# Performance work log

Measured on AMD Instinct MI355X. Metric: run time of the kernel, lower is better.

Reference implementation:

```python
import jax, jax.numpy as jnp
import numpy as np
from jax import lax

ALPHA = 2.0          # HausdorffDistanceLoss alpha
W_CE, W_BD, W_HD = 1.0, 0.5, 0.5   # combined-loss weights
NOSEED = 1e4         # sentinel 1D distance for lines with no seed pixel (>> max real distance)


def _sq_dt_binary(seed):
    """Exact squared 1D distance (along last axis) to nearest True pixel. seed: [..., L] bool."""
    L = seed.shape[-1]
    idx = jnp.arange(L, dtype=jnp.int32)
    left = lax.cummax(jnp.where(seed, idx, -1), axis=seed.ndim - 1)
    right = lax.cummin(jnp.where(seed, idx, 2 * L), axis=seed.ndim - 1, reverse=True)
    dl = jnp.where(left >= 0, (idx - left).astype(jnp.float32), jnp.float32(NOSEED))
    dr = jnp.where(right < 2 * L, (right - idx).astype(jnp.float32), jnp.float32(NOSEED))
    d = jnp.minimum(dl, dr)
    return d * d


def _sq_dt_general(f):
    """d[j] = min_y f[..., y] + (j - y)^2 along last axis (lower envelope, brute force via scan)."""
    L = f.shape[-1]
    idx = jnp.arange(L, dtype=f.dtype)
    fm = jnp.moveaxis(f, -1, 0)  # [L, ...]
    def step(carry, inp):
        fy, y = inp
        cand = fy[..., None] + (idx - y) ** 2  # [..., L]
        return jnp.minimum(carry, cand), None
    init = jnp.full(f.shape, jnp.float32(1e18), f.dtype)
    d, _ = lax.scan(step, init, (fm, idx))
    return d


def edt(seed):
    """Exact 2D Euclidean distance to nearest True pixel. seed: [..., H, W] bool.
    Equivalent to scipy.ndimage.distance_transform_edt(~seed)... i.e. scipy's
    distance_transform_edt(m) == edt(m == 0)."""
    g = jnp.swapaxes(_sq_dt_binary(jnp.swapaxes(seed, -1, -2)), -1, -2)  # pass along H
    return jnp.sqrt(_sq_dt_general(g))  # pass along W


def setup_inputs() -> dict:
    key = jax.random.key(0)
    k1, k2 = jax.random.split(key)
    pred = jax.random.normal(k1, (8, 4, 256, 256), dtype=jnp.float32)
    target = jax.random.randint(k2, (8, 256, 256), 0, 4).astype(jnp.int64)
    return {"pred": pred, "target": target}


def reference(pred, target):
    N, C, H, W = pred.shape
    tgt = target.astype(jnp.int32)

    # --- CrossEntropyLoss (mean over N,H,W) ---
    log_p = jax.nn.log_softmax(pred, axis=1)
    ce = -jnp.mean(jnp.take_along_axis(log_p, tgt[:, None, :, :], axis=1))

    p = jnp.exp(log_p)  # softmax probabilities

    # one-hot target as bool mask [N, C, H, W]
    m = tgt[:, None, :, :] == jnp.arange(C, dtype=jnp.int32)[None, :, None, None]

    # signed distance map: distance_transform_edt(~m) - distance_transform_edt(m)
    dist_to_fg = edt(m)    # == scipy distance_transform_edt(~m): dist to nearest foreground
    dist_to_bg = edt(~m)   # == scipy distance_transform_edt(m):  dist to nearest background
    signed_dm = dist_to_fg - dist_to_bg  # negative inside object

    # --- BoundaryLoss (exclude background channel 0) ---
    bd = jnp.mean(jnp.sum(p[:, 1:] * signed_dm[:, 1:], axis=(2, 3)))

    # --- HausdorffDistanceLoss (exclude background) ---
    dt_gt = dist_to_fg[:, 1:]                     # distance_transform_edt(gt_mask == 0)
    pred_seed = lax.stop_gradient(p[:, 1:]) >= 0.5  # threshold is detached in torch code
    dt_pred = edt(pred_seed)                      # distance_transform_edt(pred < 0.5)
    gt_f = m[:, 1:].astype(p.dtype)
    term1 = jnp.mean(p[:, 1:] * dt_gt ** ALPHA, axis=(2, 3))   # per (n, c) spatial means
    term2 = jnp.mean(gt_f * dt_pred ** ALPHA, axis=(2, 3))
    hd = (jnp.sum(term1) + jnp.sum(term2)) / (2 * N * (C - 1))

    total = W_CE * ce + W_BD * bd + W_HD * hd
    return total, ce, bd, hd
```

## Files before the change

kernel.cpp:

```cpp
#include <hip/hip_runtime.h>

#define NB 8
#define NC 4
#define HH 256
#define WW 256
#define HW_ (HH * WW)
#define NSL 24
#define CT 8
#define NT (WW/CT)
#define HP (HH + 1)
#define GRIDN (NSL * NT)

typedef unsigned long long u64;

__global__ __launch_bounds__(256) void k_softmax_ce(
    const float* __restrict__ pred, const int* __restrict__ tgt,
    float* __restrict__ pbuf, u64* __restrict__ rmT, u64* __restrict__ rmP,
    double* __restrict__ pce) {
  int b = blockIdx.x;
  int n = b >> 8, h = b & (HH - 1);
  int w = threadIdx.x;
  size_t base = (size_t)n * NC * HW_ + (size_t)h * WW + w;
  float x0 = pred[base];
  float x1 = pred[base + HW_];
  float x2 = pred[base + 2 * HW_];
  float x3 = pred[base + 3 * HW_];
  float mx = fmaxf(fmaxf(x0, x1), fmaxf(x2, x3));
  float e0 = __expf(x0 - mx), e1 = __expf(x1 - mx);
  float e2 = __expf(x2 - mx), e3 = __expf(x3 - mx);
  float sum = e0 + e1 + e2 + e3;
  float lse = mx + __logf(sum);
  int t = tgt[(size_t)n * HW_ + h * WW + w];
  float xt = (t == 0) ? x0 : (t == 1) ? x1 : (t == 2) ? x2 : x3;
  float ce = lse - xt;
  float inv = 1.0f / sum;
  float p1 = e1 * inv, p2 = e2 * inv, p3 = e3 * inv;
  size_t pb = ((size_t)(n * 3)) * HW_ + (size_t)h * WW + w;
  pbuf[pb]           = p1;
  pbuf[pb + HW_]     = p2;
  pbuf[pb + 2 * HW_] = p3;
  u64 bT1 = __ballot(t == 1), bP1 = __ballot(p1 >= 0.5f);
  u64 bT2 = __ballot(t == 2), bP2 = __ballot(p2 >= 0.5f);
  u64 bT3 = __ballot(t == 3), bP3 = __ballot(p3 >= 0.5f);
  int v = threadIdx.x >> 6;
  if ((threadIdx.x & 63) == 0) {
    size_t mi = ((size_t)(n * 3) * HH + h) * 4 + v;
    rmT[mi]                      = bT1;  rmP[mi]                      = bP1;
    rmT[mi + (size_t)HH * 4]     = bT2;  rmP[mi + (size_t)HH * 4]     = bP2;
    rmT[mi + (size_t)2 * HH * 4] = bT3;  rmP[mi + (size_t)2 * HH * 4] = bP3;
  }
  double cd = (double)ce;
  #pragma unroll
  for (int o = 32; o > 0; o >>= 1) cd += __shfl_down(cd, o, 64);
  if ((threadIdx.x & 63) == 0) pce[(b << 2) | v] = cd;
}

template<int WORD>
__device__ __forceinline__ int nsb_left(u64 m0, u64 m1, u64 m2, u64 m3, int bit) {
  u64 cur = (WORD == 0) ? m0 : (WORD == 1) ? m1 : (WORD == 2) ? m2 : m3;
  u64 below = cur & ((bit == 63) ? ~0ull : ((1ull << (bit + 1)) - 1ull));
  if (below) return bit - (63 - (int)__builtin_clzll(below));
  if constexpr (WORD >= 1) {
    u64 x = (WORD == 1) ? m0 : (WORD == 2) ? m1 : m2;
    if (x) return bit + 1 + (int)__builtin_clzll(x);
  }
  if constexpr (WORD >= 2) {
    u64 x = (WORD == 2) ? m0 : m1;
    if (x) return bit + 65 + (int)__builtin_clzll(x);
  }
  if constexpr (WORD >= 3) {
    if (m0) return bit + 129 + (int)__builtin_clzll(m0);
  }
  return 10000;
}

template<int WORD>
__device__ __forceinline__ int nsb_right(u64 m0, u64 m1, u64 m2, u64 m3, int bit) {
  u64 cur = (WORD == 0) ? m0 : (WORD == 1) ? m1 : (WORD == 2) ? m2 : m3;
  u64 above = cur & (~0ull << bit);
  if (above) return (int)__builtin_ctzll(above) - bit;
  if constexpr (WORD <= 2) {
    u64 x = (WORD == 0) ? m1 : (WORD == 1) ? m2 : m3;
    if (x) return 64 + (int)__builtin_ctzll(x) - bit;
  }
  if constexpr (WORD <= 1) {
    u64 x = (WORD == 0) ? m2 : m3;
    if (x) return 128 + (int)__builtin_ctzll(x) - bit;
  }
  if constexpr (WORD == 0) {
    if (m3) return 192 + (int)__builtin_ctzll(m3) - bit;
  }
  return 10000;
}

template<int WORD>
__device__ __forceinline__ void filltile(
    u64 t0, u64 t1, u64 t2, u64 t3, u64 p0, u64 p1, u64 p2, u64 p3,
    int h, int bit0, float gF[CT][HP], float gB[CT][HP], float gQ[CT][HP],
    unsigned char gtb[CT][HH + 4]) {
  u64 b0 = ~t0, b1 = ~t1, b2 = ~t2, b3 = ~t3;
  u64 curT = (WORD == 0) ? t0 : (WORD == 1) ? t1 : (WORD == 2) ? t2 : t3;
  u64 curP = (WORD == 0) ? p0 : (WORD == 1) ? p1 : (WORD == 2) ? p2 : p3;
  int dF[CT], dB[CT], dQ[CT];
  int lF = nsb_left<WORD>(t0, t1, t2, t3, bit0);
  int lB = nsb_left<WORD>(b0, b1, b2, b3, bit0);
  int lP = nsb_left<WORD>(p0, p1, p2, p3, bit0);
  #pragma unroll
  for (int wi = 0; wi < CT; ++wi) {
    int bit = bit0 + wi;
    int sF = (int)((curT >> bit) & 1ull);
    int sP = (int)((curP >> bit) & 1ull);
    if (wi > 0) {
      lF = sF ? 0 : min(lF + 1, 10000);
      lB = sF ? min(lB + 1, 10000) : 0;
      lP = sP ? 0 : min(lP + 1, 10000);
    }
    dF[wi] = lF; dB[wi] = lB; dQ[wi] = lP;
  }
  int rF = nsb_right<WORD>(t0, t1, t2, t3, bit0 + CT - 1);
  int rB = nsb_right<WORD>(b0, b1, b2, b3, bit0 + CT - 1);
  int rP = nsb_right<WORD>(p0, p1, p2, p3, bit0 + CT - 1);
  #pragma unroll
  for (int wi = CT - 1; wi >= 0; --wi) {
    int bit = bit0 + wi;
    int sF = (int)((curT >> bit) & 1ull);
    int sP = (int)((curP >> bit) & 1ull);
    if (wi < CT - 1) {
      rF = sF ? 0 : min(rF + 1, 10000);
      rB = sF ? min(rB + 1, 10000) : 0;
      rP = sP ? 0 : min(rP + 1, 10000);
    }
    int vF = min(dF[wi], rF), vB = min(dB[wi], rB), vQ = min(dQ[wi], rP);
    gF[wi][h] = (float)(vF * vF);
    gB[wi][h] = (float)(vB * vB);
    gQ[wi][h] = (float)(vQ * vQ);
    gtb[wi][h] = (unsigned char)sF;
  }
}

__global__ __launch_bounds__(256) void k_env(
    const u64* __restrict__ rmT, const u64* __restrict__ rmP,
    const float* __restrict__ pbuf, double* __restrict__ part) {
  __shared__ float gF[CT][HP];
  __shared__ float gB[CT][HP];
  __shared__ float gQ[CT][HP];
  __shared__ float pp[CT][HP];
  __shared__ unsigned char gtb[CT][HH + 4];
  __shared__ double sbuf[12];
  int tid = threadIdx.x;
  int s  = blockIdx.x;
  int w0 = blockIdx.y * CT;
  int h  = tid;
  {
    size_t mi = ((size_t)s * HH + h) * 4;
    const ulonglong2* pT = (const ulonglong2*)(rmT + mi);
    const ulonglong2* pP = (const ulonglong2*)(rmP + mi);
    ulonglong2 a0 = pT[0], a1 = pT[1];
    ulonglong2 c0 = pP[0], c1 = pP[1];
    const float* prow = pbuf + (size_t)s * HW_ + (size_t)h * WW + w0;
    float4 pa = *(const float4*)prow;
    float4 pc = *(const float4*)(prow + 4);
    pp[0][h] = pa.x; pp[1][h] = pa.y; pp[2][h] = pa.z; pp[3][h] = pa.w;
    pp[4][h] = pc.x; pp[5][h] = pc.y; pp[6][h] = pc.z; pp[7][h] = pc.w;
    int bit0 = w0 & 63;
    switch (w0 >> 6) {
      case 0: filltile<0>(a0.x,a0.y,a1.x,a1.y,c0.x,c0.y,c1.x,c1.y,h,bit0,gF,gB,gQ,gtb); break;
      case 1: filltile<1>(a0.x,a0.y,a1.x,a1.y,c0.x,c0.y,c1.x,c1.y,h,bit0,gF,gB,gQ,gtb); break;
      case 2: filltile<2>(a0.x,a0.y,a1.x,a1.y,c0.x,c0.y,c1.x,c1.y,h,bit0,gF,gB,gQ,gtb); break;
      default: filltile<3>(a0.x,a0.y,a1.x,a1.y,c0.x,c0.y,c1.x,c1.y,h,bit0,gF,gB,gQ,gtb); break;
    }
  }
  __syncthreads();
  int wi = tid & (CT - 1);
  int hg = tid >> 3;
  double a_bd = 0.0, a_t1 = 0.0, a_t2 = 0.0;
  for (int k = 0; k < 8; ++k) {
    int h2 = hg * 8 + k;
    float mF = gF[wi][h2], mB = gB[wi][h2], mQ = gQ[wi][h2];
    for (int r = 1; r < HH; r += 4) {
      float rr = (float)(r * r);
      if (rr >= mF && rr >= mB && rr >= mQ) break;
      #pragma unroll
      for (int q = 0; q < 4; ++q) {
        int rq = r + q;
        float rrq = (float)(rq * rq);
        int u = h2 - rq, d = h2 + rq;
        if (u >= 0) {
          float fF = gF[wi][u], fB = gB[wi][u], fQ = gQ[wi][u];
          mF = fminf(mF, fF + rrq);
          mB = fminf(mB, fB + rrq);
          mQ = fminf(mQ, fQ + rrq);
        }
        if (d < HH) {
          float fF = gF[wi][d], fB = gB[wi][d], fQ = gQ[wi][d];
          mF = fminf(mF, fF + rrq);
          mB = fminf(mB, fB + rrq);
          mQ = fminf(mQ, fQ + rrq);
        }
      }
    }
    float dfg = sqrtf(mF), dbg = sqrtf(mB), dpr = sqrtf(mQ);
    float p  = pp[wi][h2];
    float gt = (float)gtb[wi][h2];
    a_bd += (double)(p * (dfg - dbg));
    a_t1 += (double)(p * dfg * dfg);
    a_t2 += (double)(gt * dpr * dpr);
  }
  int lane = tid & 63, wid = tid >> 6;
  #pragma unroll
  for (int o = 32; o > 0; o >>= 1) {
    a_bd += __shfl_down(a_bd, o, 64);
    a_t1 += __shfl_down(a_t1, o, 64);
    a_t2 += __shfl_down(a_t2, o, 64);
  }
  if (lane == 0) { sbuf[wid*3] = a_bd; sbuf[wid*3+1] = a_t1; sbuf[wid*3+2] = a_t2; }
  __syncthreads();
  if (tid == 0) {
    double b = 0, t1 = 0, t2 = 0;
    #pragma unroll
    for (int i = 0; i < 4; ++i) { b += sbuf[i*3]; t1 += sbuf[i*3+1]; t2 += sbuf[i*3+2]; }
    size_t pi = ((size_t)s * NT + blockIdx.y) * 4;
    part[pi] = b; part[pi+1] = t1; part[pi+2] = t2;
  }
}

__global__ __launch_bounds__(256) void k_final(const double* __restrict__ pce,
    const double* __restrict__ part, float* __restrict__ out) {
  __shared__ double sb[16];
  int t = threadIdx.x;
  double ce = 0.0, bd = 0.0, t1 = 0.0, t2 = 0.0;
  for (int i = t; i < NB * HH * 4; i += 256) ce += pce[i];
  for (int i = t; i < NSL * NT; i += 256) {
    bd += part[(size_t)i * 4];
    t1 += part[(size_t)i * 4 + 1];
    t2 += part[(size_t)i * 4 + 2];
  }
  int lane = t & 63, wid = t >> 6;
  #pragma unroll
  for (int o = 32; o > 0; o >>= 1) {
    ce += __shfl_down(ce, o, 64);
    bd += __shfl_down(bd, o, 64);
    t1 += __shfl_down(t1, o, 64);
    t2 += __shfl_down(t2, o, 64);
  }
  if (lane == 0) { sb[wid*4]=ce; sb[wid*4+1]=bd; sb[wid*4+2]=t1; sb[wid*4+3]=t2; }
  __syncthreads();
  if (t == 0) {
    double c = 0, b = 0, u1 = 0, u2 = 0;
    #pragma unroll
    for (int i = 0; i < 4; ++i) { c += sb[i*4]; b += sb[i*4+1]; u1 += sb[i*4+2]; u2 += sb[i*4+3]; }
    c /= (double)(NB * HW_);
    b /= (double)NSL;
    double hd = (u1 + u2) / ((double)HW_ * (double)(2 * NB * (NC - 1)));
    out[0] = (float)(c + 0.5 * b + 0.5 * hd);
    out[1] = (float)c;
    out[2] = (float)b;
    out[3] = (float)hd;
  }
}

extern "C" void kernel_launch(void* const* d_in, const int* in_sizes, int n_in,
                              void* d_out, int out_size, void* d_ws, size_t ws_size,
                              hipStream_t stream) {
  (void)in_sizes; (void)n_in; (void)out_size; (void)ws_size;
  const float* pred = (const float*)d_in[0];
  const int*   tgt  = (const int*)d_in[1];
  float* out = (float*)d_out;
  char* ws = (char*)d_ws;
  double* pce  = (double*)ws;
  double* part = (double*)(ws + 65536);
  float*  pbuf = (float*)(ws + 131072);
  u64* rmT = (u64*)(ws + 131072 + (size_t)NSL * HW_ * 4);
  u64* rmP = rmT + (size_t)NSL * HH * 4;

  hipLaunchKernelGGL(k_softmax_ce, dim3(NB * HH), dim3(256), 0, stream,
                     pred, tgt, pbuf, rmT, rmP, pce);
  hipLaunchKernelGGL(k_env, dim3(NSL, NT), dim3(256), 0, stream,
                     rmT, rmP, pbuf, part);
  hipLaunchKernelGGL(k_final, dim3(1), dim3(256), 0, stream, pce, part, out);
}
```

Baseline: 89.26 us.

## Use 512 threads in envelope kernel with 4-row register tiling and split fill

The envelope kernel now launches 512 threads per block instead of 256. The fill stage splits the target-mask and prediction-mask distance computations across the two thread halves. In the envelope pass each thread handles 4 adjacent rows at once and loads a 7-element window of neighbours per radius step into registers, so each shared-memory load is reused across rows. The early break now waits for all 4 rows to be finished, which can add some extra iterations, and the register arrays raise register pressure.

```diff
diff --git a/kernel.cpp b/kernel.cpp
--- a/kernel.cpp
+++ b/kernel.cpp
@@ -94,51 +94,66 @@
 }
 
 template<int WORD>
-__device__ __forceinline__ void filltile(
-    u64 t0, u64 t1, u64 t2, u64 t3, u64 p0, u64 p1, u64 p2, u64 p3,
-    int h, int bit0, float gF[CT][HP], float gB[CT][HP], float gQ[CT][HP],
-    unsigned char gtb[CT][HH + 4]) {
+__device__ __forceinline__ void filltileT(
+    u64 t0, u64 t1, u64 t2, u64 t3, int h, int bit0,
+    float gF[CT][HP], float gB[CT][HP], unsigned char gtb[CT][HH + 4]) {
   u64 b0 = ~t0, b1 = ~t1, b2 = ~t2, b3 = ~t3;
   u64 curT = (WORD == 0) ? t0 : (WORD == 1) ? t1 : (WORD == 2) ? t2 : t3;
-  u64 curP = (WORD == 0) ? p0 : (WORD == 1) ? p1 : (WORD == 2) ? p2 : p3;
-  int dF[CT], dB[CT], dQ[CT];
+  int dF[CT], dB[CT];
   int lF = nsb_left<WORD>(t0, t1, t2, t3, bit0);
   int lB = nsb_left<WORD>(b0, b1, b2, b3, bit0);
-  int lP = nsb_left<WORD>(p0, p1, p2, p3, bit0);
   #pragma unroll
   for (int wi = 0; wi < CT; ++wi) {
     int bit = bit0 + wi;
     int sF = (int)((curT >> bit) & 1ull);
-    int sP = (int)((curP >> bit) & 1ull);
     if (wi > 0) {
       lF = sF ? 0 : min(lF + 1, 10000);
       lB = sF ? min(lB + 1, 10000) : 0;
-      lP = sP ? 0 : min(lP + 1, 10000);
-    }
-    dF[wi] = lF; dB[wi] = lB; dQ[wi] = lP;
+    }
+    dF[wi] = lF; dB[wi] = lB;
   }
   int rF = nsb_right<WORD>(t0, t1, t2, t3, bit0 + CT - 1);
   int rB = nsb_right<WORD>(b0, b1, b2, b3, bit0 + CT - 1);
-  int rP = nsb_right<WORD>(p0, p1, p2, p3, bit0 + CT - 1);
   #pragma unroll
   for (int wi = CT - 1; wi >= 0; --wi) {
     int bit = bit0 + wi;
     int sF = (int)((curT >> bit) & 1ull);
-    int sP = (int)((curP >> bit) & 1ull);
     if (wi < CT - 1) {
       rF = sF ? 0 : min(rF + 1, 10000);
       rB = sF ? min(rB + 1, 10000) : 0;
-      rP = sP ? 0 : min(rP + 1, 10000);
-    }
-    int vF = min(dF[wi], rF), vB = min(dB[wi], rB), vQ = min(dQ[wi], rP);
+    }
+    int vF = min(dF[wi], rF), vB = min(dB[wi], rB);
     gF[wi][h] = (float)(vF * vF);
     gB[wi][h] = (float)(vB * vB);
+    gtb[wi][h] = (unsigned char)sF;
+  }
+}
+
+template<int WORD>
+__device__ __forceinline__ void filltileP(
+    u64 p0, u64 p1, u64 p2, u64 p3, int h, int bit0, float gQ[CT][HP]) {
+  u64 curP = (WORD == 0) ? p0 : (WORD == 1) ? p1 : (WORD == 2) ? p2 : p3;
+  int dQ[CT];
+  int lP = nsb_left<WORD>(p0, p1, p2, p3, bit0);
+  #pragma unroll
+  for (int wi = 0; wi < CT; ++wi) {
+    int bit = bit0 + wi;
+    int sP = (int)((curP >> bit) & 1ull);
+    if (wi > 0) lP = sP ? 0 : min(lP + 1, 10000);
+    dQ[wi] = lP;
+  }
+  int rP = nsb_right<WORD>(p0, p1, p2, p3, bit0 + CT - 1);
+  #pragma unroll
+  for (int wi = CT - 1; wi >= 0; --wi) {
+    int bit = bit0 + wi;
+    int sP = (int)((curP >> bit) & 1ull);
+    if (wi < CT - 1) rP = sP ? 0 : min(rP + 1, 10000);
+    int vQ = min(dQ[wi], rP);
     gQ[wi][h] = (float)(vQ * vQ);
-    gtb[wi][h] = (unsigned char)sF;
-  }
-}
-
-__global__ __launch_bounds__(256) void k_env(
+  }
+}
+
+__global__ __launch_bounds__(512) void k_env(
     const u64* __restrict__ rmT, const u64* __restrict__ rmP,
     const float* __restrict__ pbuf, double* __restrict__ part) {
   __shared__ float gF[CT][HP];
@@ -146,60 +161,90 @@
   __shared__ float gQ[CT][HP];
   __shared__ float pp[CT][HP];
   __shared__ unsigned char gtb[CT][HH + 4];
-  __shared__ double sbuf[12];
+  __shared__ double sbuf[24];
   int tid = threadIdx.x;
   int s  = blockIdx.x;
   int w0 = blockIdx.y * CT;
-  int h  = tid;
-  {
+  int h  = tid & 255;
+  int bit0 = w0 & 63;
+  if (tid < 256) {
     size_t mi = ((size_t)s * HH + h) * 4;
     const ulonglong2* pT = (const ulonglong2*)(rmT + mi);
+    ulonglong2 a0 = pT[0], a1 = pT[1];
+    switch (w0 >> 6) {
+      case 0: filltileT<0>(a0.x, a0.y, a1.x, a1.y, h, bit0, gF, gB, gtb); break;
+      case 1: filltileT<1>(a0.x, a0.y, a1.x, a1.y, h, bit0, gF, gB, gtb); break;
+      case 2: filltileT<2>(a0.x, a0.y, a1.x, a1.y, h, bit0, gF, gB, gtb); break;
+      default: filltileT<3>(a0.x, a0.y, a1.x, a1.y, h, bit0, gF, gB, gtb); break;
+    }
+  } else {
+    size_t mi = ((size_t)s * HH + h) * 4;
     const ulonglong2* pP = (const ulonglong2*)(rmP + mi);
-    ulonglong2 a0 = pT[0], a1 = pT[1];
     ulonglong2 c0 = pP[0], c1 = pP[1];
+    switch (w0 >> 6) {
+      case 0: filltileP<0>(c0.x, c0.y, c1.x, c1.y, h, bit0, gQ); break;
+      case 1: filltileP<1>(c0.x, c0.y, c1.x, c1.y, h, bit0, gQ); break;
+      case 2: filltileP<2>(c0.x, c0.y, c1.x, c1.y, h, bit0, gQ); break;
+      default: filltileP<3>(c0.x, c0.y, c1.x, c1.y, h, bit0, gQ); break;
+    }
     const float* prow = pbuf + (size_t)s * HW_ + (size_t)h * WW + w0;
     float4 pa = *(const float4*)prow;
     float4 pc = *(const float4*)(prow + 4);
     pp[0][h] = pa.x; pp[1][h] = pa.y; pp[2][h] = pa.z; pp[3][h] = pa.w;
     pp[4][h] = pc.x; pp[5][h] = pc.y; pp[6][h] = pc.z; pp[7][h] = pc.w;
-    int bit0 = w0 & 63;
-    switch (w0 >> 6) {
-      case 0: filltile<0>(a0.x,a0.y,a1.x,a1.y,c0.x,c0.y,c1.x,c1.y,h,bit0,gF,gB,gQ,gtb); break;
-      case 1: filltile<1>(a0.x,a0.y,a1.x,a1.y,c0.x,c0.y,c1.x,c1.y,h,bit0,gF,gB,gQ,gtb); break;
-      case 2: filltile<2>(a0.x,a0.y,a1.x,a1.y,c0.x,c0.y,c1.x,c1.y,h,bit0,gF,gB,gQ,gtb); break;
-      default: filltile<3>(a0.x,a0.y,a1.x,a1.y,c0.x,c0.y,c1.x,c1.y,h,bit0,gF,gB,gQ,gtb); break;
-    }
   }
   __syncthreads();
   int wi = tid & (CT - 1);
   int hg = tid >> 3;
-  double a_bd = 0.0, a_t1 = 0.0, a_t2 = 0.0;
-  for (int k = 0; k < 8; ++k) {
-    int h2 = hg * 8 + k;
-    float mF = gF[wi][h2], mB = gB[wi][h2], mQ = gQ[wi][h2];
-    for (int r = 1; r < HH; r += 4) {
-      float rr = (float)(r * r);
-      if (rr >= mF && rr >= mB && rr >= mQ) break;
+  int h0 = hg * 4;
+  float mF[4], mB[4], mQ[4];
+  #pragma unroll
+  for (int k = 0; k < 4; ++k) {
+    mF[k] = gF[wi][h0 + k];
+    mB[k] = gB[wi][h0 + k];
+    mQ[k] = gQ[wi][h0 + k];
+  }
+  for (int r = 1; r < HH; r += 4) {
+    float rr = (float)(r * r);
+    bool need = false;
+    #pragma unroll
+    for (int k = 0; k < 4; ++k)
+      need = need || (rr < mF[k]) || (rr < mB[k]) || (rr < mQ[k]);
+    if (!need) break;
+    float uF[7], uB[7], uQ[7], dFv[7], dBv[7], dQv[7];
+    #pragma unroll
+    for (int j = 0; j < 7; ++j) {
+      int iu = h0 - r - 3 + j;
+      int id = h0 + r + j;
+      bool vu = (iu >= 0), vd = (id < HH);
+      int cu = vu ? iu : 0, cd = vd ? id : (HH - 1);
+      uF[j]  = vu ? gF[wi][cu] : 1e30f;
+      uB[j]  = vu ? gB[wi][cu] : 1e30f;
+      uQ[j]  = vu ? gQ[wi][cu] : 1e30f;
+      dFv[j] = vd ? gF[wi][cd] : 1e30f;
+      dBv[j] = vd ? gB[wi][cd] : 1e30f;
+      dQv[j] = vd ? gQ[wi][cd] : 1e30f;
+    }
+    #pragma unroll
+    for (int k = 0; k < 4; ++k) {
       #pragma unroll
       for (int q = 0; q < 4; ++q) {
         int rq = r + q;
         float rrq = (float)(rq * rq);
-        int u = h2 - rq, d = h2 + rq;
-        if (u >= 0) {
-          float fF = gF[wi][u], fB = gB[wi][u], fQ = gQ[wi][u];
-          mF = fminf(mF, fF + rrq);
-          mB = fminf(mB, fB + rrq);
-          mQ = fminf(mQ, fQ + rrq);
-        }
-        if (d < HH) {
-          float fF = gF[wi][d], fB = gB[wi][d], fQ = gQ[wi][d];
-          mF = fminf(mF, fF + rrq);
-          mB = fminf(mB, fB + rrq);
-          mQ = fminf(mQ, fQ + rrq);
-        }
+        mF[k] = fminf(mF[k], uF[k - q + 3] + rrq);
+        mB[k] = fminf(mB[k], uB[k - q + 3] + rrq);
+        mQ[k] = fminf(mQ[k], uQ[k - q + 3] + rrq);
+        mF[k] = fminf(mF[k], dFv[k + q] + rrq);
+        mB[k] = fminf(mB[k], dBv[k + q] + rrq);
+        mQ[k] = fminf(mQ[k], dQv[k + q] + rrq);
       }
     }
-    float dfg = sqrtf(mF), dbg = sqrtf(mB), dpr = sqrtf(mQ);
+  }
+  double a_bd = 0.0, a_t1 = 0.0, a_t2 = 0.0;
+  #pragma unroll
+  for (int k = 0; k < 4; ++k) {
+    int h2 = h0 + k;
+    float dfg = sqrtf(mF[k]), dbg = sqrtf(mB[k]), dpr = sqrtf(mQ[k]);
     float p  = pp[wi][h2];
     float gt = (float)gtb[wi][h2];
     a_bd += (double)(p * (dfg - dbg));
@@ -218,7 +263,7 @@
   if (tid == 0) {
     double b = 0, t1 = 0, t2 = 0;
     #pragma unroll
-    for (int i = 0; i < 4; ++i) { b += sbuf[i*3]; t1 += sbuf[i*3+1]; t2 += sbuf[i*3+2]; }
+    for (int i = 0; i < 8; ++i) { b += sbuf[i*3]; t1 += sbuf[i*3+1]; t2 += sbuf[i*3+2]; }
     size_t pi = ((size_t)s * NT + blockIdx.y) * 4;
     part[pi] = b; part[pi+1] = t1; part[pi+2] = t2;
   }
@@ -275,7 +320,7 @@
 
   hipLaunchKernelGGL(k_softmax_ce, dim3(NB * HH), dim3(256), 0, stream,
                      pred, tgt, pbuf, rmT, rmP, pce);
-  hipLaunchKernelGGL(k_env, dim3(NSL, NT), dim3(256), 0, stream,
+  hipLaunchKernelGGL(k_env, dim3(NSL, NT), dim3(512), 0, stream,
                      rmT, rmP, pbuf, part);
   hipLaunchKernelGGL(k_final, dim3(1), dim3(256), 0, stream, pce, part, out);
 }
```

New measurement: 83.85 us. 6.1% less time.
